# Optimization experiments

Hardware: AMD Instinct MI355X
Metric: run time of the kernel (lower is better)

## Reference

```python
import jax, jax.numpy as jnp
import numpy as np

B, S, D = 2, 4096, 768
H = 12
HD = D // H  # 64


def setup_inputs() -> dict:
    key = jax.random.key(0)
    ks = jax.random.split(key, 6)
    scale = 0.02
    return {
        "x": jax.random.normal(ks[0], (B, S, D), dtype=jnp.float32),
        "w_query": jax.random.normal(ks[1], (D, D), dtype=jnp.float32) * scale,
        "w_key": jax.random.normal(ks[2], (D, D), dtype=jnp.float32) * scale,
        "w_value": jax.random.normal(ks[3], (D, D), dtype=jnp.float32) * scale,
        "w_out": jax.random.normal(ks[4], (D, D), dtype=jnp.float32) * scale,
        "b_out": jax.random.normal(ks[5], (D,), dtype=jnp.float32) * scale,
    }


def reference(x, w_query, w_key, w_value, w_out, b_out):
    b, s, d = x.shape
    # Linear(in, out) applies x @ W.T; weights here stored as [out, in]-equivalent
    # square matrices, so use x @ W.T for parity with torch semantics.
    q = (x @ w_query.T).reshape(b, s, H, HD).transpose(0, 2, 1, 3)  # [b,h,s,hd]
    k = (x @ w_key.T).reshape(b, s, H, HD).transpose(0, 2, 1, 3)
    v = (x @ w_value.T).reshape(b, s, H, HD).transpose(0, 2, 1, 3)

    scores = jnp.einsum("bhqd,bhkd->bhqk", q, k)  # [b,h,s,s]
    causal = jnp.triu(jnp.ones((s, s), dtype=bool), k=1)
    scores = jnp.where(causal, -jnp.inf, scores)
    # original scales AFTER masking: softmax(masked / sqrt(head_dim))
    att = jax.nn.softmax(scores / jnp.sqrt(jnp.float32(HD)), axis=-1)
    # dropout p=0.0 (eval) -> identity
    ctx = jnp.einsum("bhqk,bhkd->bhqd", att, v)  # [b,h,s,hd]
    ctx = ctx.transpose(0, 2, 1, 3).reshape(b, s, d)
    return ctx @ w_out.T + b_out
```

## Files before the change

### kernel.cpp

```cpp
#include <hip/hip_runtime.h>
#include <stdint.h>

typedef unsigned short u16;
typedef __attribute__((ext_vector_type(8))) short bf16x8;
typedef __attribute__((ext_vector_type(4))) float f32x4;

#define MFMA(a,b,c) __builtin_amdgcn_mfma_f32_16x16x32_bf16((a),(b),(c),0,0,0)

static constexpr int S  = 4096;
static constexpr int D  = 768;
static constexpr int H  = 12;
static constexpr int HD = 64;

__device__ __forceinline__ u16 f2b(float f){
  union { float f; unsigned u; } v; v.f = f;
  unsigned r = (v.u + 0x7fffu + ((v.u >> 16) & 1u)) >> 16;
  return (u16)r;
}

__device__ __forceinline__ unsigned pack_bf16_trunc(float a, float b){
  return __builtin_amdgcn_perm(__float_as_uint(b), __float_as_uint(a), 0x07060302u);
}

__device__ __forceinline__ void cp16(const u16* g, u16* l){
  __builtin_amdgcn_global_load_lds(
      (const __attribute__((address_space(1))) unsigned int*)g,
      (__attribute__((address_space(3))) unsigned int*)l, 16, 0, 0);
}

__device__ __forceinline__ bf16x8 quad_transpose(unsigned M0, unsigned M1,
                                                 unsigned M2, unsigned M3){
  auto r0 = __builtin_amdgcn_permlane32_swap(M0, M2, false, false);
  auto r1 = __builtin_amdgcn_permlane32_swap(M1, M3, false, false);
  auto s0 = __builtin_amdgcn_permlane16_swap(r0[0], r0[1], false, false);
  auto s1 = __builtin_amdgcn_permlane16_swap(r1[0], r1[1], false, false);
  union { unsigned u[4]; bf16x8 v; } r;
  r.u[0] = s0[0];
  r.u[1] = s1[0];
  r.u[2] = s0[1];
  r.u[3] = s1[1];
  return r.v;
}

static constexpr int NX4 = (2 * S * D) / 4;
static constexpr int NW4 = (D * D) / 4;
__global__ void castall(const float* __restrict__ x,  const float* __restrict__ wq,
                        const float* __restrict__ wk, const float* __restrict__ wv,
                        const float* __restrict__ wo,
                        u16* __restrict__ xb,  u16* __restrict__ wqb,
                        u16* __restrict__ wkb, u16* __restrict__ wvb,
                        u16* __restrict__ wob){
  int i = blockIdx.x * 256 + threadIdx.x;
  const float* s; u16* d; int off;
  if (i < NX4) { s = x; d = xb; off = i; }
  else {
    int j = i - NX4; int wsel = j / NW4; off = j - wsel * NW4;
    if (wsel >= 4) return;
    s = (wsel == 0) ? wq : (wsel == 1) ? wk : (wsel == 2) ? wv : wo;
    d = (wsel == 0) ? wqb : (wsel == 1) ? wkb : (wsel == 2) ? wvb : wob;
  }
  float4 v = ((const float4*)s)[off];
  uint2 o;
  o.x = (unsigned)f2b(v.x) | ((unsigned)f2b(v.y) << 16);
  o.y = (unsigned)f2b(v.z) | ((unsigned)f2b(v.w) << 16);
  ((uint2*)d)[off] = o;
}

__global__ __launch_bounds__(256, 2) void qkv_gemm(
    const u16* __restrict__ xb, const u16* __restrict__ wq, const u16* __restrict__ wk,
    const u16* __restrict__ wv, u16* __restrict__ Qb, u16* __restrict__ Kb, u16* __restrict__ Vt)
{
  __shared__ __align__(16) u16 As[128 * 64];
  __shared__ __align__(16) u16 Bs[128 * 64];
  const int t = threadIdx.x;
  const int mblk = blockIdx.x, nblk = blockIdx.y, z = blockIdx.z;
  const u16* W = (z == 0) ? wq : (z == 1) ? wk : wv;
  const int w = t >> 6, lane = t & 63, quad = lane >> 4, l16 = lane & 15;
  const int wr = w >> 1, wc = w & 1;
  const int l7 = l16 & 7;

  f32x4 acc[4][4];
  #pragma unroll
  for (int i = 0; i < 4; i++)
    #pragma unroll
    for (int j = 0; j < 4; j++) acc[i][j] = (f32x4){0.f, 0.f, 0.f, 0.f};

  int srow[4], schk[4];
  #pragma unroll
  for (int i = 0; i < 4; i++) {
    int s = i * 256 + t;
    srow[i] = s >> 3;
    schk[i] = (s & 7) ^ (srow[i] & 7);
  }
  const u16* gA = xb + (size_t)(mblk * 128) * D;
  const u16* gB = W  + (size_t)(nblk * 128) * D;

  for (int k0 = 0; k0 < D; k0 += 64) {
    __syncthreads();
    #pragma unroll
    for (int i = 0; i < 4; i++) {
      int s = i * 256 + t;
      cp16(gA + (size_t)srow[i] * D + k0 + schk[i] * 8, As + s * 8);
      cp16(gB + (size_t)srow[i] * D + k0 + schk[i] * 8, Bs + s * 8);
    }
    __syncthreads();
    #pragma unroll
    for (int j = 0; j < 2; j++) {
      bf16x8 af[4], bfr[4];
      #pragma unroll
      for (int mt = 0; mt < 4; mt++)
        af[mt]  = *(const bf16x8*)(As + (wr * 64 + mt * 16 + l16) * 64 + ((j * 4 + quad) ^ l7) * 8);
      #pragma unroll
      for (int nt = 0; nt < 4; nt++)
        bfr[nt] = *(const bf16x8*)(Bs + (wc * 64 + nt * 16 + l16) * 64 + ((j * 4 + quad) ^ l7) * 8);
      #pragma unroll
      for (int mt = 0; mt < 4; mt++)
        #pragma unroll
        for (int nt = 0; nt < 4; nt++)
          acc[mt][nt] = MFMA(af[mt], bfr[nt], acc[mt][nt]);
    }
  }

  const float qscale = 0.18033688011112042f;
  #pragma unroll
  for (int mt = 0; mt < 4; mt++) {
    int m0 = mblk * 128 + wr * 64 + mt * 16 + quad * 4;
    #pragma unroll
    for (int nt = 0; nt < 4; nt++) {
      int n = nblk * 128 + wc * 64 + nt * 16 + l16;
      int h = n >> 6, hd = n & 63;
      if (z == 2) {
        int b = m0 >> 12, s0 = m0 & 4095;
        u16* p = Vt + (((size_t)(b * H + h) * HD + hd)) * S + s0;
        uint2 pk;
        pk.x = (unsigned)f2b(acc[mt][nt][0]) | ((unsigned)f2b(acc[mt][nt][1]) << 16);
        pk.y = (unsigned)f2b(acc[mt][nt][2]) | ((unsigned)f2b(acc[mt][nt][3]) << 16);
        *(uint2*)p = pk;
      } else {
        u16* dst = (z == 0) ? Qb : Kb;
        float sc = (z == 0) ? qscale : 1.0f;
        #pragma unroll
        for (int r = 0; r < 4; r++) {
          int m = m0 + r; int b = m >> 12, s = m & 4095;
          dst[((size_t)(b * H + h) * S + s) * HD + hd] = f2b(acc[mt][nt][r] * sc);
        }
      }
    }
  }
}

__global__ __launch_bounds__(256, 2) void attn(
    const u16* __restrict__ Qb, const u16* __restrict__ Kb,
    const u16* __restrict__ Vt, u16* __restrict__ ctx)
{
  __shared__ __align__(16) u16 Ks[128 * 64];
  __shared__ __align__(16) u16 Vts[64 * 128];
  __shared__ float Lbuf[2][4][16];
  const int t = threadIdx.x, w = t >> 6, lane = t & 63, quad = lane >> 4, l16 = lane & 15;
  const int l7 = l16 & 7;
  const int wq = w >> 1, wk = w & 1;

  const int p   = (int)blockIdx.x;
  const int xcd = p & 7;
  const int loc = p >> 3;
  const int r_  = loc >> 5, j_ = loc & 31;
  const int u   = (r_ == 0) ? j_ : (r_ == 1) ? (63 - j_) : (64 + j_);
  const int qtile = 31 - u / 3;
  const int bh    = xcd + 8 * (u % 3);

  const int q0 = qtile * 128;
  const u16* Qh = Qb + (size_t)bh * S * HD;
  const u16* Kh = Kb + (size_t)bh * S * HD;
  const u16* Vh = Vt + (size_t)bh * S * HD;
  const int b = bh / H, h = bh % H;

  bf16x8 qf[4][2];
  #pragma unroll
  for (int qt = 0; qt < 4; qt++)
    #pragma unroll
    for (int ksh = 0; ksh < 2; ksh++)
      qf[qt][ksh] = *(const bf16x8*)(Qh + (size_t)(q0 + wq * 64 + qt * 16 + l16) * HD + ksh * 32 + quad * 8);

  f32x4 ao[4][4];
  #pragma unroll
  for (int qt = 0; qt < 4; qt++)
    #pragma unroll
    for (int co = 0; co < 4; co++) ao[qt][co] = (f32x4){0.f, 0.f, 0.f, 0.f};
  float lsum[4] = {0.f, 0.f, 0.f, 0.f};

  int krow[4], kchk[4], vrow[4], vchk[4];
  #pragma unroll
  for (int i = 0; i < 4; i++) {
    int s = i * 256 + t;
    krow[i] = s >> 3;  kchk[i] = (s & 7)  ^ (krow[i] & 7);
    vrow[i] = s >> 4;  vchk[i] = (s & 15) ^ (vrow[i] & 15);
  }

  for (int kv0 = 0; kv0 <= q0; kv0 += 128) {
    const bool diag    = (kv0 == q0);
    const bool skipall = diag && (wk > wq);
    const bool mdiag   = diag && (wk == wq);

    __syncthreads();
    #pragma unroll
    for (int i = 0; i < 4; i++) {
      int s = i * 256 + t;
      cp16(Kh + (size_t)(kv0 + krow[i]) * HD + kchk[i] * 8, Ks + s * 8);
      cp16(Vh + (size_t)vrow[i] * S + kv0 + vchk[i] * 8,    Vts + s * 8);
    }
    __syncthreads();

    if (!skipall) {
      #pragma unroll
      for (int g = 0; g < 2; g++) {
        unsigned pA[4][2], pB[4][2];
        #pragma unroll
        for (int ktL = 0; ktL < 2; ktL++) {
          const int kt  = g * 2 + ktL;
          const int krw = wk * 64 + kt * 16 + l16;
          bf16x8 kf0 = *(const bf16x8*)(Ks + krw * 64 + ((0 + quad) ^ l7) * 8);
          bf16x8 kf1 = *(const bf16x8*)(Ks + krw * 64 + ((4 + quad) ^ l7) * 8);
          #pragma unroll
          for (int qt = 0; qt < 4; qt++) {
            f32x4 s0 = (f32x4){0.f, 0.f, 0.f, 0.f};
            s0 = MFMA(kf0, qf[qt][0], s0);
            s0 = MFMA(kf1, qf[qt][1], s0);
            if (mdiag) {
              const int qoff = (qt - kt) * 16 + l16;
              #pragma unroll
              for (int r = 0; r < 4; r++)
                s0[r] = (quad * 4 + r > qoff) ? -1e30f : s0[r];
            }
            float p0 = __builtin_amdgcn_exp2f(s0[0]);
            float p1 = __builtin_amdgcn_exp2f(s0[1]);
            float p2 = __builtin_amdgcn_exp2f(s0[2]);
            float p3 = __builtin_amdgcn_exp2f(s0[3]);
            lsum[qt] += (p0 + p1) + (p2 + p3);
            pA[qt][ktL] = pack_bf16_trunc(p0, p1);
            pB[qt][ktL] = pack_bf16_trunc(p2, p3);
          }
        }
        bf16x8 pf[4];
        #pragma unroll
        for (int qt = 0; qt < 4; qt++)
          pf[qt] = quad_transpose(pA[qt][0], pB[qt][0], pA[qt][1], pB[qt][1]);
        #pragma unroll
        for (int co = 0; co < 4; co++) {
          const int vrw = co * 16 + l16;
          bf16x8 vf = *(const bf16x8*)(Vts + vrw * 128 + ((wk * 8 + g * 4 + quad) ^ (vrw & 15)) * 8);
          #pragma unroll
          for (int qt = 0; qt < 4; qt++)
            ao[qt][co] = MFMA(vf, pf[qt], ao[qt][co]);
        }
      }
    }
  }

  #pragma unroll
  for (int qt = 0; qt < 4; qt++) {
    float v = lsum[qt];
    v += __shfl_xor(v, 16, 64);
    v += __shfl_xor(v, 32, 64);
    lsum[qt] = v;
  }

  __syncthreads();
  float* red = wq ? (float*)Vts : (float*)Ks;
  if (wk == 1) {
    #pragma unroll
    for (int qt = 0; qt < 4; qt++)
      #pragma unroll
      for (int co = 0; co < 4; co++)
        *(f32x4*)(red + ((qt * 4 + co) * 64 + lane) * 4) = ao[qt][co];
    if (lane < 16) {
      #pragma unroll
      for (int qt = 0; qt < 4; qt++) Lbuf[wq][qt][lane] = lsum[qt];
    }
  }
  __syncthreads();
  if (wk == 0) {
    #pragma unroll
    for (int qt = 0; qt < 4; qt++) {
      float tot = lsum[qt] + Lbuf[wq][qt][l16];
      float inv = 1.0f / tot;
      int token = b * S + q0 + wq * 64 + qt * 16 + l16;
      #pragma unroll
      for (int co = 0; co < 4; co++) {
        f32x4 pr = *(const f32x4*)(red + ((qt * 4 + co) * 64 + lane) * 4);
        f32x4 sv = ao[qt][co] + pr;
        uint2 pk;
        pk.x = (unsigned)f2b(sv[0] * inv) | ((unsigned)f2b(sv[1] * inv) << 16);
        pk.y = (unsigned)f2b(sv[2] * inv) | ((unsigned)f2b(sv[3] * inv) << 16);
        *(uint2*)(ctx + (size_t)token * D + h * HD + co * 16 + quad * 4) = pk;
      }
    }
  }
}

__global__ __launch_bounds__(256, 2) void out_gemm(
    const u16* __restrict__ ctx, const u16* __restrict__ wo,
    const float* __restrict__ bias, float* __restrict__ out)
{
  __shared__ __align__(16) u16 As[128 * 64];
  __shared__ __align__(16) u16 Bs[128 * 64];
  const int t = threadIdx.x;
  const int mblk = blockIdx.x, nblk = blockIdx.y;
  const int w = t >> 6, lane = t & 63, quad = lane >> 4, l16 = lane & 15;
  const int wr = w >> 1, wc = w & 1;
  const int l7 = l16 & 7;

  f32x4 acc[4][4];
  #pragma unroll
  for (int i = 0; i < 4; i++)
    #pragma unroll
    for (int j = 0; j < 4; j++) acc[i][j] = (f32x4){0.f, 0.f, 0.f, 0.f};

  int srow[4], schk[4];
  #pragma unroll
  for (int i = 0; i < 4; i++) {
    int s = i * 256 + t;
    srow[i] = s >> 3;
    schk[i] = (s & 7) ^ (srow[i] & 7);
  }
  const u16* gA = ctx + (size_t)(mblk * 128) * D;
  const u16* gB = wo  + (size_t)(nblk * 128) * D;

  for (int k0 = 0; k0 < D; k0 += 64) {
    __syncthreads();
    #pragma unroll
    for (int i = 0; i < 4; i++) {
      int s = i * 256 + t;
      cp16(gA + (size_t)srow[i] * D + k0 + schk[i] * 8, As + s * 8);
      cp16(gB + (size_t)srow[i] * D + k0 + schk[i] * 8, Bs + s * 8);
    }
    __syncthreads();
    #pragma unroll
    for (int j = 0; j < 2; j++) {
      bf16x8 af[4], bfr[4];
      #pragma unroll
      for (int mt = 0; mt < 4; mt++)
        af[mt]  = *(const bf16x8*)(As + (wr * 64 + mt * 16 + l16) * 64 + ((j * 4 + quad) ^ l7) * 8);
      #pragma unroll
      for (int nt = 0; nt < 4; nt++)
        bfr[nt] = *(const bf16x8*)(Bs + (wc * 64 + nt * 16 + l16) * 64 + ((j * 4 + quad) ^ l7) * 8);
      #pragma unroll
      for (int mt = 0; mt < 4; mt++)
        #pragma unroll
        for (int nt = 0; nt < 4; nt++)
          acc[mt][nt] = MFMA(af[mt], bfr[nt], acc[mt][nt]);
    }
  }

  #pragma unroll
  for (int mt = 0; mt < 4; mt++) {
    int m0 = mblk * 128 + wr * 64 + mt * 16 + quad * 4;
    #pragma unroll
    for (int nt = 0; nt < 4; nt++) {
      int n = nblk * 128 + wc * 64 + nt * 16 + l16;
      float bv = bias[n];
      #pragma unroll
      for (int r = 0; r < 4; r++)
        out[(size_t)(m0 + r) * D + n] = acc[mt][nt][r] + bv;
    }
  }
}

extern "C" void kernel_launch(void* const* d_in, const int* in_sizes, int n_in,
                              void* d_out, int out_size, void* d_ws, size_t ws_size,
                              hipStream_t stream) {
  const float* x    = (const float*)d_in[0];
  const float* wq   = (const float*)d_in[1];
  const float* wk   = (const float*)d_in[2];
  const float* wv   = (const float*)d_in[3];
  const float* wo   = (const float*)d_in[4];
  const float* bo   = (const float*)d_in[5];
  float* out = (float*)d_out;

  u16* ws = (u16*)d_ws;
  const size_t NX = (size_t)2 * S * D;
  const size_t NW = (size_t)D * D;
  u16* xb  = ws;
  u16* wqb = ws + NX;
  u16* wkb = wqb + NW;
  u16* wvb = wkb + NW;
  u16* wob = wvb + NW;
  u16* Qb  = wob + NW;
  u16* Kb  = Qb + NX;
  u16* Vt  = Kb + NX;
  u16* ctx = xb;

  const int total4 = NX4 + 4 * NW4;
  castall<<<(total4 + 255) / 256, 256, 0, stream>>>(x, wq, wk, wv, wo, xb, wqb, wkb, wvb, wob);

  qkv_gemm<<<dim3(64, 6, 3), 256, 0, stream>>>(xb, wqb, wkb, wvb, Qb, Kb, Vt);
  attn<<<dim3(768), 256, 0, stream>>>(Qb, Kb, Vt, ctx);
  out_gemm<<<dim3(64, 6), 256, 0, stream>>>(ctx, wob, bo, out);
}
```

Before: 217.4 us.

## Load K and V fragments directly from global memory, dropping LDS staging

The attention kernel no longer stages K and V tiles through shared memory behind block barriers. Each wave now reads its own K rows and transposed-V columns straight from global memory into MFMA fragments, and leaves the KV loop early on diagonal tiles it does not need. Removing both per-iteration __syncthreads lets waves run independently. The cost is that the two query-wave pairs sharing a KV half each fetch the same data, so reuse now depends on L1/L2 hits instead of LDS. Global load latency is also exposed directly in the inner loop.

```diff
diff --git a/kernel.cpp b/kernel.cpp
--- a/kernel.cpp
+++ b/kernel.cpp
@@ -153,11 +153,9 @@
     const u16* __restrict__ Qb, const u16* __restrict__ Kb,
     const u16* __restrict__ Vt, u16* __restrict__ ctx)
 {
-  __shared__ __align__(16) u16 Ks[128 * 64];
-  __shared__ __align__(16) u16 Vts[64 * 128];
+  __shared__ float Red[2][4096];
   __shared__ float Lbuf[2][4][16];
   const int t = threadIdx.x, w = t >> 6, lane = t & 63, quad = lane >> 4, l16 = lane & 15;
-  const int l7 = l16 & 7;
   const int wq = w >> 1, wk = w & 1;
 
   const int p   = (int)blockIdx.x;
@@ -188,70 +186,53 @@
     for (int co = 0; co < 4; co++) ao[qt][co] = (f32x4){0.f, 0.f, 0.f, 0.f};
   float lsum[4] = {0.f, 0.f, 0.f, 0.f};
 
-  int krow[4], kchk[4], vrow[4], vchk[4];
-  #pragma unroll
-  for (int i = 0; i < 4; i++) {
-    int s = i * 256 + t;
-    krow[i] = s >> 3;  kchk[i] = (s & 7)  ^ (krow[i] & 7);
-    vrow[i] = s >> 4;  vchk[i] = (s & 15) ^ (vrow[i] & 15);
-  }
-
   for (int kv0 = 0; kv0 <= q0; kv0 += 128) {
-    const bool diag    = (kv0 == q0);
-    const bool skipall = diag && (wk > wq);
-    const bool mdiag   = diag && (wk == wq);
-
-    __syncthreads();
-    #pragma unroll
-    for (int i = 0; i < 4; i++) {
-      int s = i * 256 + t;
-      cp16(Kh + (size_t)(kv0 + krow[i]) * HD + kchk[i] * 8, Ks + s * 8);
-      cp16(Vh + (size_t)vrow[i] * S + kv0 + vchk[i] * 8,    Vts + s * 8);
-    }
-    __syncthreads();
-
-    if (!skipall) {
-      #pragma unroll
-      for (int g = 0; g < 2; g++) {
-        unsigned pA[4][2], pB[4][2];
-        #pragma unroll
-        for (int ktL = 0; ktL < 2; ktL++) {
-          const int kt  = g * 2 + ktL;
-          const int krw = wk * 64 + kt * 16 + l16;
-          bf16x8 kf0 = *(const bf16x8*)(Ks + krw * 64 + ((0 + quad) ^ l7) * 8);
-          bf16x8 kf1 = *(const bf16x8*)(Ks + krw * 64 + ((4 + quad) ^ l7) * 8);
-          #pragma unroll
-          for (int qt = 0; qt < 4; qt++) {
-            f32x4 s0 = (f32x4){0.f, 0.f, 0.f, 0.f};
-            s0 = MFMA(kf0, qf[qt][0], s0);
-            s0 = MFMA(kf1, qf[qt][1], s0);
-            if (mdiag) {
-              const int qoff = (qt - kt) * 16 + l16;
-              #pragma unroll
-              for (int r = 0; r < 4; r++)
-                s0[r] = (quad * 4 + r > qoff) ? -1e30f : s0[r];
-            }
-            float p0 = __builtin_amdgcn_exp2f(s0[0]);
-            float p1 = __builtin_amdgcn_exp2f(s0[1]);
-            float p2 = __builtin_amdgcn_exp2f(s0[2]);
-            float p3 = __builtin_amdgcn_exp2f(s0[3]);
-            lsum[qt] += (p0 + p1) + (p2 + p3);
-            pA[qt][ktL] = pack_bf16_trunc(p0, p1);
-            pB[qt][ktL] = pack_bf16_trunc(p2, p3);
+    const bool diag = (kv0 == q0);
+    if (diag && (wk > wq)) break;
+    const bool mdiag = diag && (wk == wq);
+
+    const u16* Kt = Kh + (size_t)(kv0 + wk * 64) * HD;
+    const u16* Vs = Vh + kv0 + wk * 64;
+
+    #pragma unroll
+    for (int g = 0; g < 2; g++) {
+      unsigned pA[4][2], pB[4][2];
+      #pragma unroll
+      for (int ktL = 0; ktL < 2; ktL++) {
+        const int kt = g * 2 + ktL;
+        const u16* kr = Kt + (size_t)(kt * 16 + l16) * HD + quad * 8;
+        bf16x8 kf0 = *(const bf16x8*)(kr);
+        bf16x8 kf1 = *(const bf16x8*)(kr + 32);
+        #pragma unroll
+        for (int qt = 0; qt < 4; qt++) {
+          f32x4 s0 = (f32x4){0.f, 0.f, 0.f, 0.f};
+          s0 = MFMA(kf0, qf[qt][0], s0);
+          s0 = MFMA(kf1, qf[qt][1], s0);
+          if (mdiag) {
+            const int qoff = (qt - kt) * 16 + l16;
+            #pragma unroll
+            for (int r = 0; r < 4; r++)
+              s0[r] = (quad * 4 + r > qoff) ? -1e30f : s0[r];
           }
+          float p0 = __builtin_amdgcn_exp2f(s0[0]);
+          float p1 = __builtin_amdgcn_exp2f(s0[1]);
+          float p2 = __builtin_amdgcn_exp2f(s0[2]);
+          float p3 = __builtin_amdgcn_exp2f(s0[3]);
+          lsum[qt] += (p0 + p1) + (p2 + p3);
+          pA[qt][ktL] = pack_bf16_trunc(p0, p1);
+          pB[qt][ktL] = pack_bf16_trunc(p2, p3);
         }
-        bf16x8 pf[4];
+      }
+      bf16x8 pf[4];
+      #pragma unroll
+      for (int qt = 0; qt < 4; qt++)
+        pf[qt] = quad_transpose(pA[qt][0], pB[qt][0], pA[qt][1], pB[qt][1]);
+      #pragma unroll
+      for (int co = 0; co < 4; co++) {
+        bf16x8 vf = *(const bf16x8*)(Vs + (size_t)(co * 16 + l16) * S + g * 32 + quad * 8);
         #pragma unroll
         for (int qt = 0; qt < 4; qt++)
-          pf[qt] = quad_transpose(pA[qt][0], pB[qt][0], pA[qt][1], pB[qt][1]);
-        #pragma unroll
-        for (int co = 0; co < 4; co++) {
-          const int vrw = co * 16 + l16;
-          bf16x8 vf = *(const bf16x8*)(Vts + vrw * 128 + ((wk * 8 + g * 4 + quad) ^ (vrw & 15)) * 8);
-          #pragma unroll
-          for (int qt = 0; qt < 4; qt++)
-            ao[qt][co] = MFMA(vf, pf[qt], ao[qt][co]);
-        }
+          ao[qt][co] = MFMA(vf, pf[qt], ao[qt][co]);
       }
     }
   }
@@ -264,8 +245,7 @@
     lsum[qt] = v;
   }
 
-  __syncthreads();
-  float* red = wq ? (float*)Vts : (float*)Ks;
+  float* red = &Red[wq][0];
   if (wk == 1) {
     #pragma unroll
     for (int qt = 0; qt < 4; qt++)
```

After: 263.1 us. 1.21x slower.
